# Kernel optimization log

Hardware: AMD Instinct MI355X
Metric: run time of the kernel (lower is better)

## Reference

```python
import jax, jax.numpy as jnp
import numpy as np

# Hardcoded skeleton graph from the source module (V=15 nodes, 28 directed edges)
_SRC = np.array([0,2,4,1,3,5,6,8,10,7,9,11,13,12,2,4,14,3,5,14,8,10,13,9,11,13,12,13])
_DST = np.array([2,4,14,3,5,14,8,10,13,9,11,13,14,13,0,2,4,1,3,5,6,8,10,7,9,11,13,14])
_V = 15

def _build_lhat():
    # PyG ChebConv norm with sym laplacian, lambda_max=2: L_hat = -D^{-1/2} A D^{-1/2}, diag 0
    A = np.zeros((_V, _V), np.float32)
    A[_DST, _SRC] = 1.0  # message flows src -> dst
    deg = A.sum(axis=1)
    dinv = np.where(deg > 0, deg ** -0.5, 0.0).astype(np.float32)
    return jnp.asarray(-(dinv[:, None] * A * dinv[None, :]))

_LHAT = _build_lhat()  # [V, V]

def _lstm_layer(xs, Wih, Whh, bih, bhh):
    # xs: [T, B, in]; torch LSTM gate order: i, f, g, o
    B = xs.shape[1]
    H = Whh.shape[1]
    b = bih + bhh
    def step(carry, xt):
        h, c = carry
        g = xt @ Wih.T + h @ Whh.T + b
        i, f, gg, o = jnp.split(g, 4, axis=-1)
        c = jax.nn.sigmoid(f) * c + jax.nn.sigmoid(i) * jnp.tanh(gg)
        h = jax.nn.sigmoid(o) * jnp.tanh(c)
        return (h, c), h
    init = (jnp.zeros((B, H), xs.dtype), jnp.zeros((B, H), xs.dtype))
    _, hs = jax.lax.scan(step, init, xs)
    return hs  # [T, B, H]

def setup_inputs() -> dict:
    key = jax.random.key(0)
    ks = jax.random.split(key, 16)
    N, C, T, V, M = 512, 3, 300, 15, 2
    H, IN, NC = 128, 45, 60
    s = 0.1
    return {
        "x1": jax.random.normal(ks[0], (N, C, T, V, M), jnp.float32),
        "x2": jax.random.normal(ks[1], (N, C, T, V, M), jnp.float32),
        "cheb_w0": jax.random.normal(ks[2], (3, 3), jnp.float32) * s,
        "cheb_w1": jax.random.normal(ks[3], (3, 3), jnp.float32) * s,
        "cheb_b": jax.random.normal(ks[4], (3,), jnp.float32) * s,
        "wih0": jax.random.normal(ks[5], (4 * H, IN), jnp.float32) * s,
        "whh0": jax.random.normal(ks[6], (4 * H, H), jnp.float32) * s,
        "bih0": jax.random.normal(ks[7], (4 * H,), jnp.float32) * s,
        "bhh0": jax.random.normal(ks[8], (4 * H,), jnp.float32) * s,
        "wih1": jax.random.normal(ks[9], (4 * H, H), jnp.float32) * s,
        "whh1": jax.random.normal(ks[10], (4 * H, H), jnp.float32) * s,
        "bih1": jax.random.normal(ks[11], (4 * H,), jnp.float32) * s,
        "bhh1": jax.random.normal(ks[12], (4 * H,), jnp.float32) * s,
        "fc_w": jax.random.normal(ks[13], (NC, H), jnp.float32) * np.sqrt(2.0 / NC).astype(np.float32),
        "fc_b": jax.random.normal(ks[14], (NC,), jnp.float32) * s,
    }

def reference(x1, x2, cheb_w0, cheb_w1, cheb_b, wih0, whh0, bih0, bhh0, wih1, whh1, bih1, bhh1, fc_w, fc_b):
    N, C, T, V, M = x1.shape
    # [N,C,T,V,M] -> [N*M*T, V, C]
    x = jnp.transpose(x1, (0, 4, 2, 3, 1)).reshape(N * M * T, V, C)
    # ChebConv K=2: out = Tx0 @ W0^T + Tx1 @ W1^T + b, Tx1 = L_hat @ x
    tx1 = jnp.einsum('ij,bjc->bic', _LHAT, x)
    x = x @ cheb_w0.T + tx1 @ cheb_w1.T + cheb_b
    # [N*M, T, V*C] -> time-major [T, N*M, V*C]
    seq = x.reshape(N * M, T, V * C).transpose(1, 0, 2)
    hs0 = _lstm_layer(seq, wih0, whh0, bih0, bhh0)
    hs1 = _lstm_layer(hs0, wih1, whh1, bih1, bhh1)
    h_last = hs1[-1]  # [N*M, 128]
    logits = h_last @ fc_w.T + fc_b
    return jax.nn.softmax(logits, axis=1)
```

## Files before the change

### kernel.cpp

```cpp
#include <hip/hip_runtime.h>
#include <hip/hip_fp16.h>

typedef _Float16 half_t;
typedef _Float16 half8 __attribute__((ext_vector_type(8)));
typedef float floatx4 __attribute__((ext_vector_type(4)));
typedef int   int4v  __attribute__((ext_vector_type(4)));

#define T_STEPS 300
#define NMB     1024
#define BS      16
#define NBLK    19

#define XT_OFF   0ULL
#define XT_BYTES ((unsigned long long)(T_STEPS*NMB + 16)*64*2)
#define HS0_OFF  (XT_OFF + XT_BYTES)
#define HS0_BYTES ((unsigned long long)(T_STEPS*NMB + 16)*128*2)
#define WCH_OFF  (HS0_OFF + HS0_BYTES)
#define WCH_BYTES (512ULL*64*2)
#define BC_OFF   (WCH_OFF + WCH_BYTES)

#define S2 0.70710678118654752f
#define QH 0.5f
#define UU 0.40824829046386302f
#define TH 0.33333333333333333f
__constant__ float LHAT[225] = {
  0,0,-S2,0,0,0,0,0,0,0,0,0,0,0,0,
  0,0,0,-S2,0,0,0,0,0,0,0,0,0,0,0,
  -S2,0,0,0,-QH,0,0,0,0,0,0,0,0,0,0,
  0,-S2,0,0,0,-QH,0,0,0,0,0,0,0,0,0,
  0,0,-QH,0,0,0,0,0,0,0,0,0,0,0,-UU,
  0,0,0,-QH,0,0,0,0,0,0,0,0,0,0,-UU,
  0,0,0,0,0,0,0,0,-S2,0,0,0,0,0,0,
  0,0,0,0,0,0,0,0,0,-S2,0,0,0,0,0,
  0,0,0,0,0,0,-S2,0,0,0,-QH,0,0,0,0,
  0,0,0,0,0,0,0,-S2,0,0,0,-QH,0,0,0,
  0,0,0,0,0,0,0,0,-QH,0,0,0,0,-UU,0,
  0,0,0,0,0,0,0,0,0,-QH,0,0,0,-UU,0,
  0,0,0,0,0,0,0,0,0,0,0,0,0,0,0,
  0,0,0,0,0,0,0,0,0,0,-UU,-UU,0,0,0,
  0,0,0,0,-UU,-UU,0,0,0,0,0,0,0,-TH,0
};

__device__ __forceinline__ float frcp(float x)  { return __builtin_amdgcn_rcpf(x); }
__device__ __forceinline__ float fsig(float x)  { return frcp(1.f + __expf(-x)); }
__device__ __forceinline__ float ftanh(float x) { return 2.f*frcp(1.f + __expf(-2.f*x)) - 1.f; }

__device__ __forceinline__ half8 load_w8(const float* p) {
  const float4* q = (const float4*)p;
  float4 a = q[0], b = q[1];
  half8 f;
  f[0]=(half_t)a.x; f[1]=(half_t)a.y; f[2]=(half_t)a.z; f[3]=(half_t)a.w;
  f[4]=(half_t)b.x; f[5]=(half_t)b.y; f[6]=(half_t)b.z; f[7]=(half_t)b.w;
  return f;
}

__device__ __forceinline__ void pin(half8& f) {
  int4v t = __builtin_bit_cast(int4v, f);
  asm volatile("" : "+v"(t));
  f = __builtin_bit_cast(half8, t);
}
__device__ __forceinline__ void pinf(floatx4& f) {
  int4v t = __builtin_bit_cast(int4v, f);
  asm volatile("" : "+v"(t));
  f = __builtin_bit_cast(floatx4, t);
}

__global__ void k_prep(const float* __restrict__ w0, const float* __restrict__ w1,
                       const float* __restrict__ cb, const float* __restrict__ wih0,
                       const float* __restrict__ bih0, const float* __restrict__ bhh0,
                       half_t* __restrict__ wcomb_h, float* __restrict__ biasc) {
  const int n = threadIdx.x;
  float wrow[45];
  #pragma unroll
  for (int i=0;i<45;i++) wrow[i] = wih0[n*45+i];
  float P[45];
  #pragma unroll
  for (int i=0;i<15;i++)
    #pragma unroll
    for (int c=0;c<3;c++) {
      float s = 0.f;
      #pragma unroll
      for (int cp=0;cp<3;cp++) s += wrow[i*3+cp]*w1[cp*3+c];
      P[i*3+c] = s;
    }
  #pragma unroll
  for (int j=0;j<15;j++)
    #pragma unroll
    for (int c=0;c<3;c++) {
      float s = 0.f;
      #pragma unroll
      for (int cp=0;cp<3;cp++) s += wrow[j*3+cp]*w0[cp*3+c];
      #pragma unroll
      for (int i=0;i<15;i++) s += LHAT[i*15+j]*P[i*3+c];
      wcomb_h[n*64 + j*3+c] = (half_t)s;
    }
  for (int k=45;k<64;k++) wcomb_h[n*64+k] = (half_t)0.f;
  float b = bih0[n] + bhh0[n];
  #pragma unroll
  for (int i=0;i<15;i++)
    #pragma unroll
    for (int cp=0;cp<3;cp++) b += wrow[i*3+cp]*cb[cp];
  biasc[n] = b;
}

__global__ void k_xpose(const float* __restrict__ x1, half_t* __restrict__ xt) {
  const int id = blockIdx.x*256 + threadIdx.x;
  const int v  = id % 15;
  const int r1 = id / 15;
  const int t  = r1 % 300;
  const int r2 = r1 / 300;
  const int c  = r2 % 3;
  const int n  = r2 / 3;
  const float2 f = ((const float2*)x1)[id];
  const size_t row = (size_t)t*NMB + n*2;
  xt[row*64     + v*3 + c] = (half_t)f.x;
  xt[(row+1)*64 + v*3 + c] = (half_t)f.y;
}

__launch_bounds__(512, 2)
__global__ void k_lstm0(const half_t* __restrict__ xt, const half_t* __restrict__ wch,
                        const float* __restrict__ biasc, const float* __restrict__ whh0,
                        half_t* __restrict__ hs0) {
  __shared__ __align__(16) half_t xs[2][BS][4][80];
  __shared__ __align__(16) half_t hr[16][4][144];
  const int tid = threadIdx.x;
  const int wave = tid>>6, lane = tid&63, quad = lane>>4, l16 = lane&15;
  const int nm0 = blockIdx.x*4;

  for (int i=tid; i<4*144; i+=512) (&hr[15][0][0])[i] = (half_t)0.f;

  half8 whhF[4][4];
  half8 wcF [4][2];
  float bias[4];
  #pragma unroll
  for (int nt=0; nt<4; nt++) {
    const int gcol = nt*128 + wave*16 + l16;
    #pragma unroll
    for (int kc=0; kc<4; kc++) { whhF[nt][kc] = load_w8(whh0 + gcol*128 + kc*32 + quad*8); pin(whhF[nt][kc]); }
    #pragma unroll
    for (int kc=0; kc<2; kc++) { wcF[nt][kc] = *(const half8*)(wch + gcol*64 + kc*32 + quad*8); pin(wcF[nt][kc]); }
    bias[nt] = biasc[gcol];
  }
  float cst = 0.f;
  floatx4 z4 = {0.f,0.f,0.f,0.f}; pinf(z4);

  const int sS = tid>>5;
  const int sR = (tid>>3)&3;
  const int sC = (tid&7)*8;

  float4 ld = *(const float4*)(xt + ((size_t)sS*NMB + nm0 + sR)*64 + sC);
  *(half8*)&xs[0][sS][sR][sC] = __builtin_bit_cast(half8, ld);
  __syncthreads();

  for (int b=0; b<NBLK; b++) {
    const int bs = b*BS, buf = b&1;
    const int cnt = (T_STEPS - bs < BS) ? (T_STEPS - bs) : BS;
    const int ngr = cnt>>2;
    if (b+1 < NBLK) {
      int tt = bs + BS + sS; if (tt > 299) tt = 299;
      ld = *(const float4*)(xt + ((size_t)tt*NMB + nm0 + sR)*64 + sC);
    }
    for (int g=0; g<ngr; g++) {
      const int s0 = g*4;
      floatx4 xp[4];
      {
        const half_t* xrow = &xs[buf][s0 + (l16&3)][l16>>2][0];
        half8 xA[2];
        #pragma unroll
        for (int kc=0; kc<2; kc++) xA[kc] = *(const half8*)(xrow + kc*32 + quad*8);
        #pragma unroll
        for (int nt=0; nt<4; nt++) {
          floatx4 a = {bias[nt],bias[nt],bias[nt],bias[nt]};
          a = __builtin_amdgcn_mfma_f32_16x16x32_f16(xA[0], wcF[nt][0], a, 0,0,0);
          a = __builtin_amdgcn_mfma_f32_16x16x32_f16(xA[1], wcF[nt][1], a, 0,0,0);
          xp[nt] = a;
        }
      }
      #pragma unroll
      for (int j=0; j<4; j++) {
        const int t = bs + s0 + j;
        if (g == 0 && j == 1 && b+1 < NBLK)
          *(half8*)&xs[buf^1][sS][sR][sC] = __builtin_bit_cast(half8, ld);

        half8 hA[4];
        const half_t* hrow = &hr[(t+15)&15][l16&3][0];
        #pragma unroll
        for (int kc=0; kc<4; kc++) hA[kc] = *(const half8*)(hrow + kc*32 + quad*8);
        floatx4 ah[4];
        #pragma unroll
        for (int nt=0; nt<4; nt++) {
          floatx4 a = z4;
          #pragma unroll
          for (int kc=0; kc<4; kc++)
            a = __builtin_amdgcn_mfma_f32_16x16x32_f16(hA[kc], whhF[nt][kc], a, 0,0,0);
          ah[nt] = a;
        }
        {
          const float gi = ah[0][quad] + xp[0][j];
          const float gf = ah[1][quad] + xp[1][j];
          const float gg = ah[2][quad] + xp[2][j];
          const float go = ah[3][quad] + xp[3][j];
          cst = fsig(gf)*cst + fsig(gi)*ftanh(gg);
          hr[t&15][quad][wave*16 + l16] = (half_t)(fsig(go)*ftanh(cst));
        }
        __syncthreads();
      }
    }
    {
      const int hS = tid>>5, hR = (tid>>3)&3, hC = (tid&7)*16;
      if (hS < cnt) {
        half8 a0 = *(const half8*)&hr[(bs+hS)&15][hR][hC];
        half8 a1 = *(const half8*)&hr[(bs+hS)&15][hR][hC+8];
        half_t* dst = hs0 + ((size_t)(bs+hS)*NMB + nm0 + hR)*128 + hC;
        *(half8*)dst = a0; *(half8*)(dst+8) = a1;
      }
    }
    __syncthreads();
  }
}

__launch_bounds__(512, 2)
__global__ void k_lstm1(const half_t* __restrict__ hs0, const float* __restrict__ wih1,
                        const float* __restrict__ whh1, const float* __restrict__ bih1,
                        const float* __restrict__ bhh1, const float* __restrict__ fcw,
                        const float* __restrict__ fcb, float* __restrict__ out) {
  __shared__ __align__(16) half_t xs[2][BS][4][144];
  __shared__ __align__(16) half_t h2[2][4][144];
  __shared__ float logits_lds[240];
  const int tid = threadIdx.x;
  const int wave = tid>>6, lane = tid&63, quad = lane>>4, l16 = lane&15;
  const int nm0 = blockIdx.x*4;
  for (int i=tid; i<2*4*144; i+=512) (&h2[0][0][0])[i] = (half_t)0.f;

  half8 wxF[4][4], whF[4][4];
  float bias[4];
  #pragma unroll
  for (int nt=0; nt<4; nt++) {
    const int gcol = nt*128 + wave*16 + l16;
    #pragma unroll
    for (int kc=0; kc<4; kc++) {
      wxF[nt][kc] = load_w8(wih1 + gcol*128 + kc*32 + quad*8); pin(wxF[nt][kc]);
      whF[nt][kc] = load_w8(whh1 + gcol*128 + kc*32 + quad*8); pin(whF[nt][kc]);
    }
    bias[nt] = bih1[gcol] + bhh1[gcol];
  }
  float cst = 0.f;
  floatx4 z4 = {0.f,0.f,0.f,0.f}; pinf(z4);

  const int sS = tid>>5;
  const int sR = (tid>>3)&3;
  const int sC = (tid&7)*16;

  float4 ld0, ld1;
  { const half_t* src = hs0 + ((size_t)sS*NMB + nm0 + sR)*128 + sC;
    ld0 = *(const float4*)src; ld1 = *(const float4*)(src+8); }
  *(half8*)&xs[0][sS][sR][sC]   = __builtin_bit_cast(half8, ld0);
  *(half8*)&xs[0][sS][sR][sC+8] = __builtin_bit_cast(half8, ld1);
  __syncthreads();

  for (int b=0; b<NBLK; b++) {
    const int bs = b*BS, buf = b&1;
    const int cnt = (T_STEPS - bs < BS) ? (T_STEPS - bs) : BS;
    const int ngr = cnt>>2;
    if (b+1 < NBLK) {
      int tt = bs + BS + sS; if (tt > 299) tt = 299;
      const half_t* src = hs0 + ((size_t)tt*NMB + nm0 + sR)*128 + sC;
      ld0 = *(const float4*)src; ld1 = *(const float4*)(src+8);
    }
    for (int g=0; g<ngr; g++) {
      const int s0 = g*4;
      floatx4 xp[4];
      {
        const half_t* xrow = &xs[buf][s0 + (l16&3)][l16>>2][0];
        half8 xA[4];
        #pragma unroll
        for (int kc=0; kc<4; kc++) xA[kc] = *(const half8*)(xrow + kc*32 + quad*8);
        #pragma unroll
        for (int nt=0; nt<4; nt++) {
          floatx4 a = {bias[nt],bias[nt],bias[nt],bias[nt]};
          #pragma unroll
          for (int kc=0; kc<4; kc++)
            a = __builtin_amdgcn_mfma_f32_16x16x32_f16(xA[kc], wxF[nt][kc], a, 0,0,0);
          xp[nt] = a;
        }
      }
      #pragma unroll
      for (int j=0; j<4; j++) {
        const int t = bs + s0 + j;
        if (g == 0 && j == 1 && b+1 < NBLK) {
          *(half8*)&xs[buf^1][sS][sR][sC]   = __builtin_bit_cast(half8, ld0);
          *(half8*)&xs[buf^1][sS][sR][sC+8] = __builtin_bit_cast(half8, ld1);
        }
        half8 hA[4];
        const half_t* hrow = &h2[t&1][l16&3][0];
        #pragma unroll
        for (int kc=0; kc<4; kc++) hA[kc] = *(const half8*)(hrow + kc*32 + quad*8);
        floatx4 ah[4];
        #pragma unroll
        for (int nt=0; nt<4; nt++) {
          floatx4 a = z4;
          #pragma unroll
          for (int kc=0; kc<4; kc++)
            a = __builtin_amdgcn_mfma_f32_16x16x32_f16(hA[kc], whF[nt][kc], a, 0,0,0);
          ah[nt] = a;
        }
        {
          const float gi = ah[0][quad] + xp[0][j];
          const float gf = ah[1][quad] + xp[1][j];
          const float gg = ah[2][quad] + xp[2][j];
          const float go = ah[3][quad] + xp[3][j];
          cst = fsig(gf)*cst + fsig(gi)*ftanh(gg);
          h2[(t+1)&1][quad][wave*16 + l16] = (half_t)(fsig(go)*ftanh(cst));
        }
        __syncthreads();
      }
    }
  }

  if (tid < 240) {
    const int r2 = tid/60, cls = tid%60;
    float s = fcb[cls];
    for (int k2=0; k2<128; k2++) s += (float)h2[0][r2][k2] * fcw[cls*128+k2];
    logits_lds[r2*60+cls] = s;
  }
  __syncthreads();
  if (tid < 4) {
    float m = -1e30f;
    for (int j=0; j<60; j++) m = fmaxf(m, logits_lds[tid*60+j]);
    float s = 0.f;
    for (int j=0; j<60; j++) s += __expf(logits_lds[tid*60+j]-m);
    const float inv = frcp(s);
    for (int j=0; j<60; j++) out[(nm0+tid)*60+j] = __expf(logits_lds[tid*60+j]-m)*inv;
  }
}

extern "C" void kernel_launch(void* const* d_in, const int* in_sizes, int n_in,
                              void* d_out, int out_size, void* d_ws, size_t ws_size,
                              hipStream_t stream) {
  const float* x1      = (const float*)d_in[0];
  const float* cheb_w0 = (const float*)d_in[2];
  const float* cheb_w1 = (const float*)d_in[3];
  const float* cheb_b  = (const float*)d_in[4];
  const float* wih0    = (const float*)d_in[5];
  const float* whh0    = (const float*)d_in[6];
  const float* bih0    = (const float*)d_in[7];
  const float* bhh0    = (const float*)d_in[8];
  const float* wih1    = (const float*)d_in[9];
  const float* whh1    = (const float*)d_in[10];
  const float* bih1    = (const float*)d_in[11];
  const float* bhh1    = (const float*)d_in[12];
  const float* fc_w    = (const float*)d_in[13];
  const float* fc_b    = (const float*)d_in[14];

  char* ws = (char*)d_ws;
  half_t* xt    = (half_t*)(ws + XT_OFF);
  half_t* hs0   = (half_t*)(ws + HS0_OFF);
  half_t* wch   = (half_t*)(ws + WCH_OFF);
  float*  biasc = (float*)(ws + BC_OFF);

  k_prep <<<dim3(1),     dim3(512), 0, stream>>>(cheb_w0, cheb_w1, cheb_b, wih0, bih0, bhh0, wch, biasc);
  k_xpose<<<dim3(27000), dim3(256), 0, stream>>>(x1, xt);
  k_lstm0<<<dim3(256),   dim3(512), 0, stream>>>(xt, wch, biasc, whh0, hs0);
  k_lstm1<<<dim3(256),   dim3(512), 0, stream>>>(hs0, wih1, whh1, bih1, bhh1, fc_w, fc_b, (float*)d_out);
}
```

Baseline: 517.9 us.

## Fuse both LSTM layers into one launch with flag-based producer/consumer pipelining

Merges the two LSTM layer kernels into a single launch of 512 workgroups. Blocks 0-255 run layer 0 and publish a per-workgroup progress flag after each 16-step chunk of hs0 is written. Blocks 256-511 run layer 1 and spin on that flag before loading the next chunk. The aim is to run layer 1 concurrently with layer 0 so the two serial recurrences overlap instead of running back to back. This depends on all 512 blocks being co-resident (launch bounds raised to 4 blocks per CU); otherwise the spin-waits could deadlock.

```diff
diff --git a/kernel.cpp b/kernel.cpp
--- a/kernel.cpp
+++ b/kernel.cpp
@@ -18,6 +18,8 @@
 #define WCH_OFF  (HS0_OFF + HS0_BYTES)
 #define WCH_BYTES (512ULL*64*2)
 #define BC_OFF   (WCH_OFF + WCH_BYTES)
+#define BC_BYTES (512ULL*4)
+#define FLAG_OFF (BC_OFF + BC_BYTES)
 
 #define S2 0.70710678118654752f
 #define QH 0.5f
@@ -65,11 +67,22 @@
   f = __builtin_bit_cast(floatx4, t);
 }
 
+__device__ __forceinline__ void wait_flag(const int* f, int want, int tid) {
+  if (tid == 0) {
+    while (__hip_atomic_load(f, __ATOMIC_RELAXED, __HIP_MEMORY_SCOPE_AGENT) < want)
+      __builtin_amdgcn_s_sleep(8);
+    (void)__hip_atomic_load(f, __ATOMIC_ACQUIRE, __HIP_MEMORY_SCOPE_AGENT);
+  }
+  __syncthreads();
+}
+
 __global__ void k_prep(const float* __restrict__ w0, const float* __restrict__ w1,
                        const float* __restrict__ cb, const float* __restrict__ wih0,
                        const float* __restrict__ bih0, const float* __restrict__ bhh0,
-                       half_t* __restrict__ wcomb_h, float* __restrict__ biasc) {
+                       half_t* __restrict__ wcomb_h, float* __restrict__ biasc,
+                       int* __restrict__ flags) {
   const int n = threadIdx.x;
+  if (n < 256) flags[n*16] = 0;
   float wrow[45];
   #pragma unroll
   for (int i=0;i<45;i++) wrow[i] = wih0[n*45+i];
@@ -117,220 +130,229 @@
   xt[(row+1)*64 + v*3 + c] = (half_t)f.y;
 }
 
-__launch_bounds__(512, 2)
-__global__ void k_lstm0(const half_t* __restrict__ xt, const half_t* __restrict__ wch,
-                        const float* __restrict__ biasc, const float* __restrict__ whh0,
-                        half_t* __restrict__ hs0) {
-  __shared__ __align__(16) half_t xs[2][BS][4][80];
-  __shared__ __align__(16) half_t hr[16][4][144];
+__launch_bounds__(512, 4)
+__global__ void k_lstm_fused(const half_t* __restrict__ xt, const half_t* __restrict__ wch,
+                             const float* __restrict__ biasc, const float* __restrict__ whh0,
+                             half_t* __restrict__ hs0,
+                             const float* __restrict__ wih1, const float* __restrict__ whh1,
+                             const float* __restrict__ bih1, const float* __restrict__ bhh1,
+                             const float* __restrict__ fcw, const float* __restrict__ fcb,
+                             float* __restrict__ out, int* __restrict__ flags) {
+  __shared__ __align__(16) char smem[40192];
   const int tid = threadIdx.x;
   const int wave = tid>>6, lane = tid&63, quad = lane>>4, l16 = lane&15;
-  const int nm0 = blockIdx.x*4;
-
-  for (int i=tid; i<4*144; i+=512) (&hr[15][0][0])[i] = (half_t)0.f;
-
-  half8 whhF[4][4];
-  half8 wcF [4][2];
-  float bias[4];
-  #pragma unroll
-  for (int nt=0; nt<4; nt++) {
-    const int gcol = nt*128 + wave*16 + l16;
-    #pragma unroll
-    for (int kc=0; kc<4; kc++) { whhF[nt][kc] = load_w8(whh0 + gcol*128 + kc*32 + quad*8); pin(whhF[nt][kc]); }
-    #pragma unroll
-    for (int kc=0; kc<2; kc++) { wcF[nt][kc] = *(const half8*)(wch + gcol*64 + kc*32 + quad*8); pin(wcF[nt][kc]); }
-    bias[nt] = biasc[gcol];
-  }
-  float cst = 0.f;
-  floatx4 z4 = {0.f,0.f,0.f,0.f}; pinf(z4);
-
-  const int sS = tid>>5;
-  const int sR = (tid>>3)&3;
-  const int sC = (tid&7)*8;
-
-  float4 ld = *(const float4*)(xt + ((size_t)sS*NMB + nm0 + sR)*64 + sC);
-  *(half8*)&xs[0][sS][sR][sC] = __builtin_bit_cast(half8, ld);
-  __syncthreads();
-
-  for (int b=0; b<NBLK; b++) {
-    const int bs = b*BS, buf = b&1;
-    const int cnt = (T_STEPS - bs < BS) ? (T_STEPS - bs) : BS;
-    const int ngr = cnt>>2;
-    if (b+1 < NBLK) {
-      int tt = bs + BS + sS; if (tt > 299) tt = 299;
-      ld = *(const float4*)(xt + ((size_t)tt*NMB + nm0 + sR)*64 + sC);
-    }
-    for (int g=0; g<ngr; g++) {
-      const int s0 = g*4;
-      floatx4 xp[4];
+
+  if (blockIdx.x < 256) {
+    auto xs = (half_t (*)[BS][4][80])smem;
+    auto hr = (half_t (*)[4][144])(smem + 20480);
+    const int wg  = blockIdx.x;
+    const int nm0 = wg*4;
+    int* flag = flags + wg*16;
+
+    for (int i=tid; i<4*144; i+=512) (&hr[15][0][0])[i] = (half_t)0.f;
+
+    half8 whhF[4][4];
+    half8 wcF [4][2];
+    float bias[4];
+    #pragma unroll
+    for (int nt=0; nt<4; nt++) {
+      const int gcol = nt*128 + wave*16 + l16;
+      #pragma unroll
+      for (int kc=0; kc<4; kc++) { whhF[nt][kc] = load_w8(whh0 + gcol*128 + kc*32 + quad*8); pin(whhF[nt][kc]); }
+      #pragma unroll
+      for (int kc=0; kc<2; kc++) { wcF[nt][kc] = *(const half8*)(wch + gcol*64 + kc*32 + quad*8); pin(wcF[nt][kc]); }
+      bias[nt] = biasc[gcol];
+    }
+    float cst = 0.f;
+    floatx4 z4 = {0.f,0.f,0.f,0.f}; pinf(z4);
+
+    const int sS = tid>>5;
+    const int sR = (tid>>3)&3;
+    const int sC = (tid&7)*8;
+
+    float4 ld = *(const float4*)(xt + ((size_t)sS*NMB + nm0 + sR)*64 + sC);
+    *(half8*)&xs[0][sS][sR][sC] = __builtin_bit_cast(half8, ld);
+    __syncthreads();
+
+    for (int b=0; b<NBLK; b++) {
+      const int bs = b*BS, buf = b&1;
+      const int cnt = (T_STEPS - bs < BS) ? (T_STEPS - bs) : BS;
+      const int ngr = cnt>>2;
+      if (b+1 < NBLK) {
+        int tt = bs + BS + sS; if (tt > 299) tt = 299;
+        ld = *(const float4*)(xt + ((size_t)tt*NMB + nm0 + sR)*64 + sC);
+      }
+      for (int g=0; g<ngr; g++) {
+        const int s0 = g*4;
+        floatx4 xp[4];
+        {
+          const half_t* xrow = &xs[buf][s0 + (l16&3)][l16>>2][0];
+          half8 xA[2];
+          #pragma unroll
+          for (int kc=0; kc<2; kc++) xA[kc] = *(const half8*)(xrow + kc*32 + quad*8);
+          #pragma unroll
+          for (int nt=0; nt<4; nt++) {
+            floatx4 a = {bias[nt],bias[nt],bias[nt],bias[nt]};
+            a = __builtin_amdgcn_mfma_f32_16x16x32_f16(xA[0], wcF[nt][0], a, 0,0,0);
+            a = __builtin_amdgcn_mfma_f32_16x16x32_f16(xA[1], wcF[nt][1], a, 0,0,0);
+            xp[nt] = a;
+          }
+        }
+        #pragma unroll
+        for (int j=0; j<4; j++) {
+          const int t = bs + s0 + j;
+          if (g == 0 && j == 1 && b+1 < NBLK)
+            *(half8*)&xs[buf^1][sS][sR][sC] = __builtin_bit_cast(half8, ld);
+
+          half8 hA[4];
+          const half_t* hrow = &hr[(t+15)&15][l16&3][0];
+          #pragma unroll
+          for (int kc=0; kc<4; kc++) hA[kc] = *(const half8*)(hrow + kc*32 + quad*8);
+          floatx4 ah[4];
+          #pragma unroll
+          for (int nt=0; nt<4; nt++) {
+            floatx4 a = z4;
+            #pragma unroll
+            for (int kc=0; kc<4; kc++)
+              a = __builtin_amdgcn_mfma_f32_16x16x32_f16(hA[kc], whhF[nt][kc], a, 0,0,0);
+            ah[nt] = a;
+          }
+          {
+            const float gi = ah[0][quad] + xp[0][j];
+            const float gf = ah[1][quad] + xp[1][j];
+            const float gg = ah[2][quad] + xp[2][j];
+            const float go = ah[3][quad] + xp[3][j];
+            cst = fsig(gf)*cst + fsig(gi)*ftanh(gg);
+            hr[t&15][quad][wave*16 + l16] = (half_t)(fsig(go)*ftanh(cst));
+          }
+          __syncthreads();
+        }
+      }
       {
-        const half_t* xrow = &xs[buf][s0 + (l16&3)][l16>>2][0];
-        half8 xA[2];
+        const int hS = tid>>5, hR = (tid>>3)&3, hC = (tid&7)*16;
+        if (hS < cnt) {
+          half8 a0 = *(const half8*)&hr[(bs+hS)&15][hR][hC];
+          half8 a1 = *(const half8*)&hr[(bs+hS)&15][hR][hC+8];
+          half_t* dst = hs0 + ((size_t)(bs+hS)*NMB + nm0 + hR)*128 + hC;
+          *(half8*)dst = a0; *(half8*)(dst+8) = a1;
+        }
+      }
+      __syncthreads();
+      if (tid == 0)
+        __hip_atomic_store(flag, b+1, __ATOMIC_RELEASE, __HIP_MEMORY_SCOPE_AGENT);
+    }
+  } else {
+    auto xs = (half_t (*)[BS][4][144])smem;
+    auto h2 = (half_t (*)[4][144])(smem + 36864);
+    float* logits_lds = (float*)(smem + 39168);
+    const int wg  = blockIdx.x - 256;
+    const int nm0 = wg*4;
+    const int* flag = flags + wg*16;
+
+    for (int i=tid; i<2*4*144; i+=512) (&h2[0][0][0])[i] = (half_t)0.f;
+
+    half8 wxF[4][4], whF[4][4];
+    float bias[4];
+    #pragma unroll
+    for (int nt=0; nt<4; nt++) {
+      const int gcol = nt*128 + wave*16 + l16;
+      #pragma unroll
+      for (int kc=0; kc<4; kc++) {
+        wxF[nt][kc] = load_w8(wih1 + gcol*128 + kc*32 + quad*8); pin(wxF[nt][kc]);
+        whF[nt][kc] = load_w8(whh1 + gcol*128 + kc*32 + quad*8); pin(whF[nt][kc]);
+      }
+      bias[nt] = bih1[gcol] + bhh1[gcol];
+    }
+    float cst = 0.f;
+    floatx4 z4 = {0.f,0.f,0.f,0.f}; pinf(z4);
+
+    const int sS = tid>>5;
+    const int sR = (tid>>3)&3;
+    const int sC = (tid&7)*16;
+
+    wait_flag(flag, 1, tid);
+    float4 ld0, ld1;
+    { const half_t* src = hs0 + ((size_t)sS*NMB + nm0 + sR)*128 + sC;
+      ld0 = *(const float4*)src; ld1 = *(const float4*)(src+8); }
+    *(half8*)&xs[0][sS][sR][sC]   = __builtin_bit_cast(half8, ld0);
+    *(half8*)&xs[0][sS][sR][sC+8] = __builtin_bit_cast(half8, ld1);
+    __syncthreads();
+
+    for (int b=0; b<NBLK; b++) {
+      const int bs = b*BS, buf = b&1;
+      const int cnt = (T_STEPS - bs < BS) ? (T_STEPS - bs) : BS;
+      const int ngr = cnt>>2;
+      if (b+1 < NBLK) {
+        wait_flag(flag, b+2, tid);
+        int tt = bs + BS + sS; if (tt > 299) tt = 299;
+        const half_t* src = hs0 + ((size_t)tt*NMB + nm0 + sR)*128 + sC;
+        ld0 = *(const float4*)src; ld1 = *(const float4*)(src+8);
+      }
+      for (int g=0; g<ngr; g++) {
+        const int s0 = g*4;
+        floatx4 xp[4];
+        {
+          const half_t* xrow = &xs[buf][s0 + (l16&3)][l16>>2][0];
+          half8 xA[4];
+          #pragma unroll
+          for (int kc=0; kc<4; kc++) xA[kc] = *(const half8*)(xrow + kc*32 + quad*8);
+          #pragma unroll
+          for (int nt=0; nt<4; nt++) {
+            floatx4 a = {bias[nt],bias[nt],bias[nt],bias[nt]};
+            #pragma unroll
+            for (int kc=0; kc<4; kc++)
+              a = __builtin_amdgcn_mfma_f32_16x16x32_f16(xA[kc], wxF[nt][kc], a, 0,0,0);
+            xp[nt] = a;
+          }
+        }
         #pragma unroll
-        for (int kc=0; kc<2; kc++) xA[kc] = *(const half8*)(xrow + kc*32 + quad*8);
-        #pragma unroll
-        for (int nt=0; nt<4; nt++) {
-          floatx4 a = {bias[nt],bias[nt],bias[nt],bias[nt]};
-          a = __builtin_amdgcn_mfma_f32_16x16x32_f16(xA[0], wcF[nt][0], a, 0,0,0);
-          a = __builtin_amdgcn_mfma_f32_16x16x32_f16(xA[1], wcF[nt][1], a, 0,0,0);
-          xp[nt] = a;
-        }
-      }
-      #pragma unroll
-      for (int j=0; j<4; j++) {
-        const int t = bs + s0 + j;
-        if (g == 0 && j == 1 && b+1 < NBLK)
-          *(half8*)&xs[buf^1][sS][sR][sC] = __builtin_bit_cast(half8, ld);
-
-        half8 hA[4];
-        const half_t* hrow = &hr[(t+15)&15][l16&3][0];
-        #pragma unroll
-        for (int kc=0; kc<4; kc++) hA[kc] = *(const half8*)(hrow + kc*32 + quad*8);
-        floatx4 ah[4];
-        #pragma unroll
-        for (int nt=0; nt<4; nt++) {
-          floatx4 a = z4;
-          #pragma unroll
-          for (int kc=0; kc<4; kc++)
-            a = __builtin_amdgcn_mfma_f32_16x16x32_f16(hA[kc], whhF[nt][kc], a, 0,0,0);
-          ah[nt] = a;
-        }
-        {
-          const float gi = ah[0][quad] + xp[0][j];
-          const float gf = ah[1][quad] + xp[1][j];
-          const float gg = ah[2][quad] + xp[2][j];
-          const float go = ah[3][quad] + xp[3][j];
-          cst = fsig(gf)*cst + fsig(gi)*ftanh(gg);
-          hr[t&15][quad][wave*16 + l16] = (half_t)(fsig(go)*ftanh(cst));
-        }
-        __syncthreads();
-      }
-    }
-    {
-      const int hS = tid>>5, hR = (tid>>3)&3, hC = (tid&7)*16;
-      if (hS < cnt) {
-        half8 a0 = *(const half8*)&hr[(bs+hS)&15][hR][hC];
-        half8 a1 = *(const half8*)&hr[(bs+hS)&15][hR][hC+8];
-        half_t* dst = hs0 + ((size_t)(bs+hS)*NMB + nm0 + hR)*128 + hC;
-        *(half8*)dst = a0; *(half8*)(dst+8) = a1;
-      }
+        for (int j=0; j<4; j++) {
+          const int t = bs + s0 + j;
+          if (g == 0 && j == 1 && b+1 < NBLK) {
+            *(half8*)&xs[buf^1][sS][sR][sC]   = __builtin_bit_cast(half8, ld0);
+            *(half8*)&xs[buf^1][sS][sR][sC+8] = __builtin_bit_cast(half8, ld1);
+          }
+          half8 hA[4];
+          const half_t* hrow = &h2[t&1][l16&3][0];
+          #pragma unroll
+          for (int kc=0; kc<4; kc++) hA[kc] = *(const half8*)(hrow + kc*32 + quad*8);
+          floatx4 ah[4];
+          #pragma unroll
+          for (int nt=0; nt<4; nt++) {
+            floatx4 a = z4;
+            #pragma unroll
+            for (int kc=0; kc<4; kc++)
+              a = __builtin_amdgcn_mfma_f32_16x16x32_f16(hA[kc], whF[nt][kc], a, 0,0,0);
+            ah[nt] = a;
+          }
+          {
+            const float gi = ah[0][quad] + xp[0][j];
+            const float gf = ah[1][quad] + xp[1][j];
+            const float gg = ah[2][quad] + xp[2][j];
+            const float go = ah[3][quad] + xp[3][j];
+            cst = fsig(gf)*cst + fsig(gi)*ftanh(gg);
+            h2[(t+1)&1][quad][wave*16 + l16] = (half_t)(fsig(go)*ftanh(cst));
+          }
+          __syncthreads();
+        }
+      }
+    }
+
+    if (tid < 240) {
+      const int r2 = tid/60, cls = tid%60;
+      float s = fcb[cls];
+      for (int k2=0; k2<128; k2++) s += (float)h2[0][r2][k2] * fcw[cls*128+k2];
+      logits_lds[r2*60+cls] = s;
     }
     __syncthreads();
-  }
-}
-
-__launch_bounds__(512, 2)
-__global__ void k_lstm1(const half_t* __restrict__ hs0, const float* __restrict__ wih1,
-                        const float* __restrict__ whh1, const float* __restrict__ bih1,
-                        const float* __restrict__ bhh1, const float* __restrict__ fcw,
-                        const float* __restrict__ fcb, float* __restrict__ out) {
-  __shared__ __align__(16) half_t xs[2][BS][4][144];
-  __shared__ __align__(16) half_t h2[2][4][144];
-  __shared__ float logits_lds[240];
-  const int tid = threadIdx.x;
-  const int wave = tid>>6, lane = tid&63, quad = lane>>4, l16 = lane&15;
-  const int nm0 = blockIdx.x*4;
-  for (int i=tid; i<2*4*144; i+=512) (&h2[0][0][0])[i] = (half_t)0.f;
-
-  half8 wxF[4][4], whF[4][4];
-  float bias[4];
-  #pragma unroll
-  for (int nt=0; nt<4; nt++) {
-    const int gcol = nt*128 + wave*16 + l16;
-    #pragma unroll
-    for (int kc=0; kc<4; kc++) {
-      wxF[nt][kc] = load_w8(wih1 + gcol*128 + kc*32 + quad*8); pin(wxF[nt][kc]);
-      whF[nt][kc] = load_w8(whh1 + gcol*128 + kc*32 + quad*8); pin(whF[nt][kc]);
-    }
-    bias[nt] = bih1[gcol] + bhh1[gcol];
-  }
-  float cst = 0.f;
-  floatx4 z4 = {0.f,0.f,0.f,0.f}; pinf(z4);
-
-  const int sS = tid>>5;
-  const int sR = (tid>>3)&3;
-  const int sC = (tid&7)*16;
-
-  float4 ld0, ld1;
-  { const half_t* src = hs0 + ((size_t)sS*NMB + nm0 + sR)*128 + sC;
-    ld0 = *(const float4*)src; ld1 = *(const float4*)(src+8); }
-  *(half8*)&xs[0][sS][sR][sC]   = __builtin_bit_cast(half8, ld0);
-  *(half8*)&xs[0][sS][sR][sC+8] = __builtin_bit_cast(half8, ld1);
-  __syncthreads();
-
-  for (int b=0; b<NBLK; b++) {
-    const int bs = b*BS, buf = b&1;
-    const int cnt = (T_STEPS - bs < BS) ? (T_STEPS - bs) : BS;
-    const int ngr = cnt>>2;
-    if (b+1 < NBLK) {
-      int tt = bs + BS + sS; if (tt > 299) tt = 299;
-      const half_t* src = hs0 + ((size_t)tt*NMB + nm0 + sR)*128 + sC;
-      ld0 = *(const float4*)src; ld1 = *(const float4*)(src+8);
-    }
-    for (int g=0; g<ngr; g++) {
-      const int s0 = g*4;
-      floatx4 xp[4];
-      {
-        const half_t* xrow = &xs[buf][s0 + (l16&3)][l16>>2][0];
-        half8 xA[4];
-        #pragma unroll
-        for (int kc=0; kc<4; kc++) xA[kc] = *(const half8*)(xrow + kc*32 + quad*8);
-        #pragma unroll
-        for (int nt=0; nt<4; nt++) {
-          floatx4 a = {bias[nt],bias[nt],bias[nt],bias[nt]};
-          #pragma unroll
-          for (int kc=0; kc<4; kc++)
-            a = __builtin_amdgcn_mfma_f32_16x16x32_f16(xA[kc], wxF[nt][kc], a, 0,0,0);
-          xp[nt] = a;
-        }
-      }
-      #pragma unroll
-      for (int j=0; j<4; j++) {
-        const int t = bs + s0 + j;
-        if (g == 0 && j == 1 && b+1 < NBLK) {
-          *(half8*)&xs[buf^1][sS][sR][sC]   = __builtin_bit_cast(half8, ld0);
-          *(half8*)&xs[buf^1][sS][sR][sC+8] = __builtin_bit_cast(half8, ld1);
-        }
-        half8 hA[4];
-        const half_t* hrow = &h2[t&1][l16&3][0];
-        #pragma unroll
-        for (int kc=0; kc<4; kc++) hA[kc] = *(const half8*)(hrow + kc*32 + quad*8);
-        floatx4 ah[4];
-        #pragma unroll
-        for (int nt=0; nt<4; nt++) {
-          floatx4 a = z4;
-          #pragma unroll
-          for (int kc=0; kc<4; kc++)
-            a = __builtin_amdgcn_mfma_f32_16x16x32_f16(hA[kc], whF[nt][kc], a, 0,0,0);
-          ah[nt] = a;
-        }
-        {
-          const float gi = ah[0][quad] + xp[0][j];
-          const float gf = ah[1][quad] + xp[1][j];
-          const float gg = ah[2][quad] + xp[2][j];
-          const float go = ah[3][quad] + xp[3][j];
-          cst = fsig(gf)*cst + fsig(gi)*ftanh(gg);
-          h2[(t+1)&1][quad][wave*16 + l16] = (half_t)(fsig(go)*ftanh(cst));
-        }
-        __syncthreads();
-      }
-    }
-  }
-
-  if (tid < 240) {
-    const int r2 = tid/60, cls = tid%60;
-    float s = fcb[cls];
-    for (int k2=0; k2<128; k2++) s += (float)h2[0][r2][k2] * fcw[cls*128+k2];
-    logits_lds[r2*60+cls] = s;
-  }
-  __syncthreads();
-  if (tid < 4) {
-    float m = -1e30f;
-    for (int j=0; j<60; j++) m = fmaxf(m, logits_lds[tid*60+j]);
-    float s = 0.f;
-    for (int j=0; j<60; j++) s += __expf(logits_lds[tid*60+j]-m);
-    const float inv = frcp(s);
-    for (int j=0; j<60; j++) out[(nm0+tid)*60+j] = __expf(logits_lds[tid*60+j]-m)*inv;
+    if (tid < 4) {
+      float m = -1e30f;
+      for (int j=0; j<60; j++) m = fmaxf(m, logits_lds[tid*60+j]);
+      float s = 0.f;
+      for (int j=0; j<60; j++) s += __expf(logits_lds[tid*60+j]-m);
+      const float inv = frcp(s);
+      for (int j=0; j<60; j++) out[(nm0+tid)*60+j] = __expf(logits_lds[tid*60+j]-m)*inv;
+    }
   }
 }
 
@@ -357,9 +379,10 @@
   half_t* hs0   = (half_t*)(ws + HS0_OFF);
   half_t* wch   = (half_t*)(ws + WCH_OFF);
   float*  biasc = (float*)(ws + BC_OFF);
-
-  k_prep <<<dim3(1),     dim3(512), 0, stream>>>(cheb_w0, cheb_w1, cheb_b, wih0, bih0, bhh0, wch, biasc);
+  int*    flags = (int*)(ws + FLAG_OFF);
+
+  k_prep <<<dim3(1),     dim3(512), 0, stream>>>(cheb_w0, cheb_w1, cheb_b, wih0, bih0, bhh0, wch, biasc, flags);
   k_xpose<<<dim3(27000), dim3(256), 0, stream>>>(x1, xt);
-  k_lstm0<<<dim3(256),   dim3(512), 0, stream>>>(xt, wch, biasc, whh0, hs0);
-  k_lstm1<<<dim3(256),   dim3(512), 0, stream>>>(hs0, wih1, whh1, bih1, bhh1, fc_w, fc_b, (float*)d_out);
-}
+  k_lstm_fused<<<dim3(512), dim3(512), 0, stream>>>(
+      xt, wch, biasc, whh0, hs0, wih1, whh1, bih1, bhh1, fc_w, fc_b, (float*)d_out, flags);
+}
```

After: 1.204 ms. 2.33x slower.

## Fuse both LSTM layers into one wavefront-pipelined kernel, drop hs0 buffer

Applied to the files above, without the earlier changes.

Merges the two LSTM layer kernels into a single kernel. Each loop iteration advances layer 0 at step i and layer 1 at step i-1, exchanging hidden states through double-buffered shared memory. This removes the global round trip of the layer-0 hidden sequence and one kernel launch. The layer-0 bias is folded into the Chebyshev input weights through a constant-one input column. The input projection weights now live in LDS instead of registers, so they are re-read every step, and the occupancy bound drops to one block per CU. The per-timestep x projection is no longer batched four steps ahead, so each sequential step does more serial work.

```diff
diff --git a/kernel.cpp b/kernel.cpp
--- a/kernel.cpp
+++ b/kernel.cpp
@@ -8,16 +8,10 @@
 
 #define T_STEPS 300
 #define NMB     1024
-#define BS      16
-#define NBLK    19
 
 #define XT_OFF   0ULL
 #define XT_BYTES ((unsigned long long)(T_STEPS*NMB + 16)*64*2)
-#define HS0_OFF  (XT_OFF + XT_BYTES)
-#define HS0_BYTES ((unsigned long long)(T_STEPS*NMB + 16)*128*2)
-#define WCH_OFF  (HS0_OFF + HS0_BYTES)
-#define WCH_BYTES (512ULL*64*2)
-#define BC_OFF   (WCH_OFF + WCH_BYTES)
+#define WCH_OFF  (XT_OFF + XT_BYTES)
 
 #define S2 0.70710678118654752f
 #define QH 0.5f
@@ -68,7 +62,7 @@
 __global__ void k_prep(const float* __restrict__ w0, const float* __restrict__ w1,
                        const float* __restrict__ cb, const float* __restrict__ wih0,
                        const float* __restrict__ bih0, const float* __restrict__ bhh0,
-                       half_t* __restrict__ wcomb_h, float* __restrict__ biasc) {
+                       half_t* __restrict__ wcomb_h) {
   const int n = threadIdx.x;
   float wrow[45];
   #pragma unroll
@@ -94,13 +88,13 @@
       for (int i=0;i<15;i++) s += LHAT[i*15+j]*P[i*3+c];
       wcomb_h[n*64 + j*3+c] = (half_t)s;
     }
-  for (int k=45;k<64;k++) wcomb_h[n*64+k] = (half_t)0.f;
   float b = bih0[n] + bhh0[n];
   #pragma unroll
   for (int i=0;i<15;i++)
     #pragma unroll
     for (int cp=0;cp<3;cp++) b += wrow[i*3+cp]*cb[cp];
-  biasc[n] = b;
+  wcomb_h[n*64 + 45] = (half_t)b;
+  for (int k=46;k<64;k++) wcomb_h[n*64+k] = (half_t)0.f;
 }
 
 __global__ void k_xpose(const float* __restrict__ x1, half_t* __restrict__ xt) {
@@ -115,222 +109,153 @@
   const size_t row = (size_t)t*NMB + n*2;
   xt[row*64     + v*3 + c] = (half_t)f.x;
   xt[(row+1)*64 + v*3 + c] = (half_t)f.y;
-}
-
-__launch_bounds__(512, 2)
-__global__ void k_lstm0(const half_t* __restrict__ xt, const half_t* __restrict__ wch,
-                        const float* __restrict__ biasc, const float* __restrict__ whh0,
-                        half_t* __restrict__ hs0) {
-  __shared__ __align__(16) half_t xs[2][BS][4][80];
-  __shared__ __align__(16) half_t hr[16][4][144];
+  if (c==0 && v==0) {
+    #pragma unroll
+    for (int k=45;k<64;k++) {
+      const half_t z = (half_t)((k==45)?1.f:0.f);
+      xt[row*64+k] = z; xt[(row+1)*64+k] = z;
+    }
+  }
+}
+
+__launch_bounds__(512, 1)
+__global__ void k_lstm_m(const half_t* __restrict__ xt, const half_t* __restrict__ wch,
+                         const float* __restrict__ whh0, const float* __restrict__ wih1,
+                         const float* __restrict__ whh1, const float* __restrict__ bih1,
+                         const float* __restrict__ bhh1, const float* __restrict__ fcw,
+                         const float* __restrict__ fcb, float* __restrict__ out) {
+  __shared__ __align__(16) half_t wcl[512][72];
+  __shared__ __align__(16) half_t xr[2][4][64];
+  __shared__ __align__(16) half_t hr[2][4][144];
+  __shared__ __align__(16) half_t h2[2][4][144];
+  __shared__ float logits[240];
   const int tid = threadIdx.x;
   const int wave = tid>>6, lane = tid&63, quad = lane>>4, l16 = lane&15;
+  const int colw = wave*16 + l16;
   const int nm0 = blockIdx.x*4;
 
-  for (int i=tid; i<4*144; i+=512) (&hr[15][0][0])[i] = (half_t)0.f;
-
-  half8 whhF[4][4];
-  half8 wcF [4][2];
-  float bias[4];
+  {
+    const float4* s = (const float4*)(wch + tid*64);
+    float4* d = (float4*)&wcl[tid][0];
+    #pragma unroll
+    for (int k=0;k<8;k++) d[k] = s[k];
+  }
+  for (int i=tid; i<2*4*144; i+=512) { (&hr[0][0][0])[i] = (half_t)0.f; (&h2[0][0][0])[i] = (half_t)0.f; }
+
+  half8 whhF[4][4], wxF[4][4], whF[4][4]; float bias1[4];
   #pragma unroll
   for (int nt=0; nt<4; nt++) {
-    const int gcol = nt*128 + wave*16 + l16;
-    #pragma unroll
-    for (int kc=0; kc<4; kc++) { whhF[nt][kc] = load_w8(whh0 + gcol*128 + kc*32 + quad*8); pin(whhF[nt][kc]); }
-    #pragma unroll
-    for (int kc=0; kc<2; kc++) { wcF[nt][kc] = *(const half8*)(wch + gcol*64 + kc*32 + quad*8); pin(wcF[nt][kc]); }
-    bias[nt] = biasc[gcol];
-  }
-  float cst = 0.f;
+    const int gcol = nt*128 + colw;
+    #pragma unroll
+    for (int kc=0; kc<4; kc++) {
+      whhF[nt][kc] = load_w8(whh0 + gcol*128 + kc*32 + quad*8); pin(whhF[nt][kc]);
+      wxF [nt][kc] = load_w8(wih1 + gcol*128 + kc*32 + quad*8); pin(wxF [nt][kc]);
+      whF [nt][kc] = load_w8(whh1 + gcol*128 + kc*32 + quad*8); pin(whF [nt][kc]);
+    }
+    bias1[nt] = bih1[gcol] + bhh1[gcol];
+  }
   floatx4 z4 = {0.f,0.f,0.f,0.f}; pinf(z4);
-
-  const int sS = tid>>5;
-  const int sR = (tid>>3)&3;
-  const int sC = (tid&7)*8;
-
-  float4 ld = *(const float4*)(xt + ((size_t)sS*NMB + nm0 + sR)*64 + sC);
-  *(half8*)&xs[0][sS][sR][sC] = __builtin_bit_cast(half8, ld);
+  float cst0 = 0.f, cst1 = 0.f;
+
+  float4 xldr;
+  if (wave==0 && lane<32) {
+    float4 a = *(const float4*)(xt + (size_t)nm0*64 + lane*8);
+    xldr     = *(const float4*)(xt + ((size_t)1*NMB + nm0)*64 + lane*8);
+    *(float4*)((half_t*)&xr[0][0][0] + lane*8) = a;
+  }
   __syncthreads();
 
-  for (int b=0; b<NBLK; b++) {
-    const int bs = b*BS, buf = b&1;
-    const int cnt = (T_STEPS - bs < BS) ? (T_STEPS - bs) : BS;
-    const int ngr = cnt>>2;
-    if (b+1 < NBLK) {
-      int tt = bs + BS + sS; if (tt > 299) tt = 299;
-      ld = *(const float4*)(xt + ((size_t)tt*NMB + nm0 + sR)*64 + sC);
-    }
-    for (int g=0; g<ngr; g++) {
-      const int s0 = g*4;
-      floatx4 xp[4];
-      {
-        const half_t* xrow = &xs[buf][s0 + (l16&3)][l16>>2][0];
-        half8 xA[2];
-        #pragma unroll
-        for (int kc=0; kc<2; kc++) xA[kc] = *(const half8*)(xrow + kc*32 + quad*8);
-        #pragma unroll
-        for (int nt=0; nt<4; nt++) {
-          floatx4 a = {bias[nt],bias[nt],bias[nt],bias[nt]};
-          a = __builtin_amdgcn_mfma_f32_16x16x32_f16(xA[0], wcF[nt][0], a, 0,0,0);
-          a = __builtin_amdgcn_mfma_f32_16x16x32_f16(xA[1], wcF[nt][1], a, 0,0,0);
-          xp[nt] = a;
-        }
-      }
-      #pragma unroll
-      for (int j=0; j<4; j++) {
-        const int t = bs + s0 + j;
-        if (g == 0 && j == 1 && b+1 < NBLK)
-          *(half8*)&xs[buf^1][sS][sR][sC] = __builtin_bit_cast(half8, ld);
-
-        half8 hA[4];
-        const half_t* hrow = &hr[(t+15)&15][l16&3][0];
-        #pragma unroll
-        for (int kc=0; kc<4; kc++) hA[kc] = *(const half8*)(hrow + kc*32 + quad*8);
-        floatx4 ah[4];
-        #pragma unroll
-        for (int nt=0; nt<4; nt++) {
-          floatx4 a = z4;
-          #pragma unroll
-          for (int kc=0; kc<4; kc++)
-            a = __builtin_amdgcn_mfma_f32_16x16x32_f16(hA[kc], whhF[nt][kc], a, 0,0,0);
-          ah[nt] = a;
-        }
-        {
-          const float gi = ah[0][quad] + xp[0][j];
-          const float gf = ah[1][quad] + xp[1][j];
-          const float gg = ah[2][quad] + xp[2][j];
-          const float go = ah[3][quad] + xp[3][j];
-          cst = fsig(gf)*cst + fsig(gi)*ftanh(gg);
-          hr[t&15][quad][wave*16 + l16] = (half_t)(fsig(go)*ftanh(cst));
-        }
-        __syncthreads();
-      }
-    }
-    {
-      const int hS = tid>>5, hR = (tid>>3)&3, hC = (tid&7)*16;
-      if (hS < cnt) {
-        half8 a0 = *(const half8*)&hr[(bs+hS)&15][hR][hC];
-        half8 a1 = *(const half8*)&hr[(bs+hS)&15][hR][hC+8];
-        half_t* dst = hs0 + ((size_t)(bs+hS)*NMB + nm0 + hR)*128 + hC;
-        *(half8*)dst = a0; *(half8*)(dst+8) = a1;
-      }
+  for (int i=0; i<=T_STEPS; i++) {
+    const int cur = i&1, nxt = cur^1;
+    if (i < T_STEPS) {
+      if (wave==0 && lane<32) {
+        if (i <= T_STEPS-2) *(float4*)((half_t*)&xr[nxt][0][0] + lane*8) = xldr;
+        if (i <= T_STEPS-3) xldr = *(const float4*)(xt + ((size_t)(i+2)*NMB + nm0)*64 + lane*8);
+      }
+      floatx4 xp0[4];
+      {
+        const half_t* xrow = &xr[cur][l16&3][0];
+        half8 xa0 = *(const half8*)(xrow + quad*8);
+        half8 xa1 = *(const half8*)(xrow + 32 + quad*8);
+        #pragma unroll
+        for (int nt=0; nt<4; nt++) {
+          const half_t* wr = &wcl[nt*128 + colw][0];
+          half8 w0 = *(const half8*)(wr + quad*8);
+          half8 w1 = *(const half8*)(wr + 32 + quad*8);
+          floatx4 a = __builtin_amdgcn_mfma_f32_16x16x32_f16(xa0, w0, z4, 0,0,0);
+          xp0[nt]   = __builtin_amdgcn_mfma_f32_16x16x32_f16(xa1, w1, a, 0,0,0);
+        }
+      }
+      floatx4 ah[4];
+      {
+        const half_t* hrow = &hr[nxt][l16&3][0];
+        half8 ha[4];
+        #pragma unroll
+        for (int kc=0; kc<4; kc++) ha[kc] = *(const half8*)(hrow + kc*32 + quad*8);
+        #pragma unroll
+        for (int nt=0; nt<4; nt++) {
+          floatx4 a = __builtin_amdgcn_mfma_f32_16x16x32_f16(ha[0], whhF[nt][0], xp0[nt], 0,0,0);
+          a = __builtin_amdgcn_mfma_f32_16x16x32_f16(ha[1], whhF[nt][1], a, 0,0,0);
+          a = __builtin_amdgcn_mfma_f32_16x16x32_f16(ha[2], whhF[nt][2], a, 0,0,0);
+          ah[nt] = __builtin_amdgcn_mfma_f32_16x16x32_f16(ha[3], whhF[nt][3], a, 0,0,0);
+        }
+      }
+      cst0 = fsig(ah[1][quad])*cst0 + fsig(ah[0][quad])*ftanh(ah[2][quad]);
+      hr[cur][quad][colw] = (half_t)(fsig(ah[3][quad])*ftanh(cst0));
+    }
+    if (i >= 1) {
+      floatx4 xp1[4];
+      {
+        const half_t* hx = &hr[nxt][l16&3][0];
+        half8 xb[4];
+        #pragma unroll
+        for (int kc=0; kc<4; kc++) xb[kc] = *(const half8*)(hx + kc*32 + quad*8);
+        #pragma unroll
+        for (int nt=0; nt<4; nt++) {
+          floatx4 a = __builtin_amdgcn_mfma_f32_16x16x32_f16(xb[0], wxF[nt][0], z4, 0,0,0);
+          a = __builtin_amdgcn_mfma_f32_16x16x32_f16(xb[1], wxF[nt][1], a, 0,0,0);
+          a = __builtin_amdgcn_mfma_f32_16x16x32_f16(xb[2], wxF[nt][2], a, 0,0,0);
+          xp1[nt] = __builtin_amdgcn_mfma_f32_16x16x32_f16(xb[3], wxF[nt][3], a, 0,0,0);
+        }
+      }
+      floatx4 bh[4];
+      {
+        const half_t* h1r = &h2[nxt][l16&3][0];
+        half8 hb[4];
+        #pragma unroll
+        for (int kc=0; kc<4; kc++) hb[kc] = *(const half8*)(h1r + kc*32 + quad*8);
+        #pragma unroll
+        for (int nt=0; nt<4; nt++) {
+          floatx4 a = __builtin_amdgcn_mfma_f32_16x16x32_f16(hb[0], whF[nt][0], xp1[nt], 0,0,0);
+          a = __builtin_amdgcn_mfma_f32_16x16x32_f16(hb[1], whF[nt][1], a, 0,0,0);
+          a = __builtin_amdgcn_mfma_f32_16x16x32_f16(hb[2], whF[nt][2], a, 0,0,0);
+          bh[nt] = __builtin_amdgcn_mfma_f32_16x16x32_f16(hb[3], whF[nt][3], a, 0,0,0);
+        }
+      }
+      const float gi = bh[0][quad] + bias1[0];
+      const float gf = bh[1][quad] + bias1[1];
+      const float gg = bh[2][quad] + bias1[2];
+      const float go = bh[3][quad] + bias1[3];
+      cst1 = fsig(gf)*cst1 + fsig(gi)*ftanh(gg);
+      h2[cur][quad][colw] = (half_t)(fsig(go)*ftanh(cst1));
     }
     __syncthreads();
   }
-}
-
-__launch_bounds__(512, 2)
-__global__ void k_lstm1(const half_t* __restrict__ hs0, const float* __restrict__ wih1,
-                        const float* __restrict__ whh1, const float* __restrict__ bih1,
-                        const float* __restrict__ bhh1, const float* __restrict__ fcw,
-                        const float* __restrict__ fcb, float* __restrict__ out) {
-  __shared__ __align__(16) half_t xs[2][BS][4][144];
-  __shared__ __align__(16) half_t h2[2][4][144];
-  __shared__ float logits_lds[240];
-  const int tid = threadIdx.x;
-  const int wave = tid>>6, lane = tid&63, quad = lane>>4, l16 = lane&15;
-  const int nm0 = blockIdx.x*4;
-  for (int i=tid; i<2*4*144; i+=512) (&h2[0][0][0])[i] = (half_t)0.f;
-
-  half8 wxF[4][4], whF[4][4];
-  float bias[4];
-  #pragma unroll
-  for (int nt=0; nt<4; nt++) {
-    const int gcol = nt*128 + wave*16 + l16;
-    #pragma unroll
-    for (int kc=0; kc<4; kc++) {
-      wxF[nt][kc] = load_w8(wih1 + gcol*128 + kc*32 + quad*8); pin(wxF[nt][kc]);
-      whF[nt][kc] = load_w8(whh1 + gcol*128 + kc*32 + quad*8); pin(whF[nt][kc]);
-    }
-    bias[nt] = bih1[gcol] + bhh1[gcol];
-  }
-  float cst = 0.f;
-  floatx4 z4 = {0.f,0.f,0.f,0.f}; pinf(z4);
-
-  const int sS = tid>>5;
-  const int sR = (tid>>3)&3;
-  const int sC = (tid&7)*16;
-
-  float4 ld0, ld1;
-  { const half_t* src = hs0 + ((size_t)sS*NMB + nm0 + sR)*128 + sC;
-    ld0 = *(const float4*)src; ld1 = *(const float4*)(src+8); }
-  *(half8*)&xs[0][sS][sR][sC]   = __builtin_bit_cast(half8, ld0);
-  *(half8*)&xs[0][sS][sR][sC+8] = __builtin_bit_cast(half8, ld1);
-  __syncthreads();
-
-  for (int b=0; b<NBLK; b++) {
-    const int bs = b*BS, buf = b&1;
-    const int cnt = (T_STEPS - bs < BS) ? (T_STEPS - bs) : BS;
-    const int ngr = cnt>>2;
-    if (b+1 < NBLK) {
-      int tt = bs + BS + sS; if (tt > 299) tt = 299;
-      const half_t* src = hs0 + ((size_t)tt*NMB + nm0 + sR)*128 + sC;
-      ld0 = *(const float4*)src; ld1 = *(const float4*)(src+8);
-    }
-    for (int g=0; g<ngr; g++) {
-      const int s0 = g*4;
-      floatx4 xp[4];
-      {
-        const half_t* xrow = &xs[buf][s0 + (l16&3)][l16>>2][0];
-        half8 xA[4];
-        #pragma unroll
-        for (int kc=0; kc<4; kc++) xA[kc] = *(const half8*)(xrow + kc*32 + quad*8);
-        #pragma unroll
-        for (int nt=0; nt<4; nt++) {
-          floatx4 a = {bias[nt],bias[nt],bias[nt],bias[nt]};
-          #pragma unroll
-          for (int kc=0; kc<4; kc++)
-            a = __builtin_amdgcn_mfma_f32_16x16x32_f16(xA[kc], wxF[nt][kc], a, 0,0,0);
-          xp[nt] = a;
-        }
-      }
-      #pragma unroll
-      for (int j=0; j<4; j++) {
-        const int t = bs + s0 + j;
-        if (g == 0 && j == 1 && b+1 < NBLK) {
-          *(half8*)&xs[buf^1][sS][sR][sC]   = __builtin_bit_cast(half8, ld0);
-          *(half8*)&xs[buf^1][sS][sR][sC+8] = __builtin_bit_cast(half8, ld1);
-        }
-        half8 hA[4];
-        const half_t* hrow = &h2[t&1][l16&3][0];
-        #pragma unroll
-        for (int kc=0; kc<4; kc++) hA[kc] = *(const half8*)(hrow + kc*32 + quad*8);
-        floatx4 ah[4];
-        #pragma unroll
-        for (int nt=0; nt<4; nt++) {
-          floatx4 a = z4;
-          #pragma unroll
-          for (int kc=0; kc<4; kc++)
-            a = __builtin_amdgcn_mfma_f32_16x16x32_f16(hA[kc], whF[nt][kc], a, 0,0,0);
-          ah[nt] = a;
-        }
-        {
-          const float gi = ah[0][quad] + xp[0][j];
-          const float gf = ah[1][quad] + xp[1][j];
-          const float gg = ah[2][quad] + xp[2][j];
-          const float go = ah[3][quad] + xp[3][j];
-          cst = fsig(gf)*cst + fsig(gi)*ftanh(gg);
-          h2[(t+1)&1][quad][wave*16 + l16] = (half_t)(fsig(go)*ftanh(cst));
-        }
-        __syncthreads();
-      }
-    }
-  }
 
   if (tid < 240) {
-    const int r2 = tid/60, cls = tid%60;
+    const int rr = tid/60, cls = tid%60;
     float s = fcb[cls];
-    for (int k2=0; k2<128; k2++) s += (float)h2[0][r2][k2] * fcw[cls*128+k2];
-    logits_lds[r2*60+cls] = s;
+    for (int k2=0; k2<128; k2++) s += (float)h2[0][rr][k2] * fcw[cls*128+k2];
+    logits[rr*60+cls] = s;
   }
   __syncthreads();
   if (tid < 4) {
     float m = -1e30f;
-    for (int j=0; j<60; j++) m = fmaxf(m, logits_lds[tid*60+j]);
+    for (int j=0; j<60; j++) m = fmaxf(m, logits[tid*60+j]);
     float s = 0.f;
-    for (int j=0; j<60; j++) s += __expf(logits_lds[tid*60+j]-m);
+    for (int j=0; j<60; j++) s += __expf(logits[tid*60+j]-m);
     const float inv = frcp(s);
-    for (int j=0; j<60; j++) out[(nm0+tid)*60+j] = __expf(logits_lds[tid*60+j]-m)*inv;
+    for (int j=0; j<60; j++) out[(nm0+tid)*60+j] = __expf(logits[tid*60+j]-m)*inv;
   }
 }
 
@@ -353,13 +278,11 @@
   const float* fc_b    = (const float*)d_in[14];
 
   char* ws = (char*)d_ws;
-  half_t* xt    = (half_t*)(ws + XT_OFF);
-  half_t* hs0   = (half_t*)(ws + HS0_OFF);
-  half_t* wch   = (half_t*)(ws + WCH_OFF);
-  float*  biasc = (float*)(ws + BC_OFF);
-
-  k_prep <<<dim3(1),     dim3(512), 0, stream>>>(cheb_w0, cheb_w1, cheb_b, wih0, bih0, bhh0, wch, biasc);
+  half_t* xt  = (half_t*)(ws + XT_OFF);
+  half_t* wch = (half_t*)(ws + WCH_OFF);
+
+  k_prep <<<dim3(1),     dim3(512), 0, stream>>>(cheb_w0, cheb_w1, cheb_b, wih0, bih0, bhh0, wch);
   k_xpose<<<dim3(27000), dim3(256), 0, stream>>>(x1, xt);
-  k_lstm0<<<dim3(256),   dim3(512), 0, stream>>>(xt, wch, biasc, whh0, hs0);
-  k_lstm1<<<dim3(256),   dim3(512), 0, stream>>>(hs0, wih1, whh1, bih1, bhh1, fc_w, fc_b, (float*)d_out);
-}
+  k_lstm_m<<<dim3(256),  dim3(512), 0, stream>>>(
+      xt, wch, whh0, wih1, whh1, bih1, bhh1, fc_w, fc_b, (float*)d_out);
+}
```

Measured after the change: 631.9 us. 1.22x slower.
